# Optimization experiments

Measured on AMD Instinct MI355X. Metric: run time of the kernel, lower is better.

The kernel has to match this reference:

```python
import jax, jax.numpy as jnp
import numpy as np

BASE_TEMP, MIN_TEMP, MAX_TEMP = 0.07, 0.04, 0.2
B, D = 4096, 768


def setup_inputs() -> dict:
    key = jax.random.key(0)
    k1, k2, k3 = jax.random.split(key, 3)
    return {
        "vision_features": jax.random.normal(k1, (B, D), dtype=jnp.float32),
        "text_features": jax.random.normal(k2, (B, D), dtype=jnp.float32),
        "match_ids": jax.random.randint(k3, (B,), 0, 1024, dtype=jnp.int64),
    }


def reference(vision_features, text_features, match_ids):
    # L2-normalize features along the feature dim
    v = vision_features / jnp.linalg.norm(vision_features, axis=1, keepdims=True)
    t = text_features / jnp.linalg.norm(text_features, axis=1, keepdims=True)
    sim = v @ t.T  # [B, B]

    n = match_ids.shape[0]
    match = match_ids[:, None] == match_ids[None, :]  # [B, B] bool, diag True
    mf = match.astype(sim.dtype)
    eye = jnp.eye(n, dtype=sim.dtype)
    pos_mask = mf * (1.0 - eye)          # diagonal zeroed
    neg_mask = 1.0 - mf                   # diagonal also zero (was match)

    pos_mean = (pos_mask * sim).sum() / jnp.maximum(1.0, pos_mask.sum())
    neg_mean = (neg_mask * sim).sum() / jnp.maximum(1.0, neg_mask.sum())
    separation = pos_mean - neg_mean
    temp = jnp.clip(BASE_TEMP * (0.8 + 0.4 * jnp.exp(-2.0 * separation)),
                    MIN_TEMP, MAX_TEMP)

    logits = sim / temp
    # v2t: for each row i, sum over positives j of (-logits[i,j] + lse(row i))
    lse_rows = jax.nn.logsumexp(logits, axis=1)  # [B]
    v2t = (mf * (lse_rows[:, None] - logits)).sum()
    # t2v: for each column i, sum over positives j of (-logits[j,i] + lse(col i))
    lse_cols = jax.nn.logsumexp(logits, axis=0)  # [B]
    t2v = (mf * (lse_cols[None, :] - logits)).sum()

    num_pos = mf.sum()  # includes diagonal, matching the torch code
    v2t = v2t / num_pos
    t2v = t2v / num_pos
    loss = (v2t + t2v) / 2.0
    return loss
```

## Files before the change

### kernel.cpp

```cpp
#include <hip/hip_runtime.h>
#include <hip/hip_bf16.h>

#define NB 4096
#define DD 768
#define NKT 24
#define NBLK 256

typedef __bf16 bf16x8 __attribute__((ext_vector_type(8)));
typedef float f32x4 __attribute__((ext_vector_type(4)));
typedef unsigned int uint;

#define WAITVM(N) asm volatile("s_waitcnt vmcnt(" #N ")" ::: "memory")
#define WAITLGKM0 asm volatile("s_waitcnt lgkmcnt(0)" ::: "memory")

__global__ void init_kernel(float* scal)
{
    if (threadIdx.x < 16) scal[threadIdx.x] = 0.0f;
}

__device__ __forceinline__ void stage_range(
    __hip_bfloat16* ldsAll,
    const __hip_bfloat16* __restrict__ vhat, const __hip_bfloat16* __restrict__ that_,
    int rowBase, int colBase, int T, int i0, int i1, int wid, int lane)
{
    int u = T & 3;
    int k0 = T * 32;
    const __hip_bfloat16* src = (wid >= 4) ? that_ : vhat;
    int tb = (wid >= 4) ? colBase : rowBase;
    int w4 = wid & 3;
    int logc = (lane & 3) ^ ((lane >> 3) & 3);
    int rowIn = w4 * 64 + (lane >> 2);
    __hip_bfloat16* dbase = ldsAll + u * 16384 + ((wid >= 4) ? 8192 : 0) + w4 * 2048;
    #pragma unroll
    for (int i = i0; i <= i1; ++i) {
        const __hip_bfloat16* g = src + (size_t)(tb + rowIn + i * 16) * DD + k0 + logc * 8;
        __builtin_amdgcn_global_load_lds(
            (const __attribute__((address_space(1))) void*)g,
            (__attribute__((address_space(3))) void*)(dbase + i * 512),
            16, 0, 0);
    }
}

__global__ __launch_bounds__(512, 2) void fused_kernel(
    const float* __restrict__ vf, const float* __restrict__ tf, const int* __restrict__ ids,
    __hip_bfloat16* __restrict__ vhat, __hip_bfloat16* __restrict__ that_,
    float* scal, float* rs, float* cs, float* cntf, int* npart, uint* bar,
    float* __restrict__ out)
{
    __shared__ __hip_bfloat16 ldsAll[4 * 16384];
    __shared__ int idr[256], idc[256];
    __shared__ float red[24];
    __shared__ float rs_l[256], cs_l[256];
    __shared__ int bp[16], wred_i[8];
    __shared__ float ra[8], rn[8];
    __shared__ float invT_sh, mf_sh;

    int rawb = blockIdx.x;
    int t = threadIdx.x, wid = t >> 6, lane = t & 63;

    #pragma unroll
    for (int it = 0; it < 4; ++it) {
        int row = rawb * 32 + wid * 4 + it;
        const float* src;
        __hip_bfloat16* dst;
        if (row < NB) { src = vf + (size_t)row * DD; dst = vhat + (size_t)row * DD; }
        else          { src = tf + (size_t)(row - NB) * DD; dst = that_ + (size_t)(row - NB) * DD; }
        float4 x0 = *(const float4*)(src + lane * 4);
        float4 x1 = *(const float4*)(src + 256 + lane * 4);
        float4 x2 = *(const float4*)(src + 512 + lane * 4);
        float s = x0.x*x0.x + x0.y*x0.y + x0.z*x0.z + x0.w*x0.w
                + x1.x*x1.x + x1.y*x1.y + x1.z*x1.z + x1.w*x1.w
                + x2.x*x2.x + x2.y*x2.y + x2.z*x2.z + x2.w*x2.w;
        #pragma unroll
        for (int off = 1; off < 64; off <<= 1) s += __shfl_xor(s, off, 64);
        float scale = 1.0f / sqrtf(s);
        unsigned short* dsh = (unsigned short*)dst;
        ushort4 o0, o1, o2;
        o0.x = __builtin_bit_cast(unsigned short, __float2bfloat16(x0.x * scale));
        o0.y = __builtin_bit_cast(unsigned short, __float2bfloat16(x0.y * scale));
        o0.z = __builtin_bit_cast(unsigned short, __float2bfloat16(x0.z * scale));
        o0.w = __builtin_bit_cast(unsigned short, __float2bfloat16(x0.w * scale));
        o1.x = __builtin_bit_cast(unsigned short, __float2bfloat16(x1.x * scale));
        o1.y = __builtin_bit_cast(unsigned short, __float2bfloat16(x1.y * scale));
        o1.z = __builtin_bit_cast(unsigned short, __float2bfloat16(x1.z * scale));
        o1.w = __builtin_bit_cast(unsigned short, __float2bfloat16(x1.w * scale));
        o2.x = __builtin_bit_cast(unsigned short, __float2bfloat16(x2.x * scale));
        o2.y = __builtin_bit_cast(unsigned short, __float2bfloat16(x2.y * scale));
        o2.z = __builtin_bit_cast(unsigned short, __float2bfloat16(x2.z * scale));
        o2.w = __builtin_bit_cast(unsigned short, __float2bfloat16(x2.w * scale));
        *(ushort4*)(dsh + lane * 4)       = o0;
        *(ushort4*)(dsh + 256 + lane * 4) = o1;
        *(ushort4*)(dsh + 512 + lane * 4) = o2;
    }

    int* idsh = (int*)ldsAll;
    for (int i = t; i < NB; i += 512) idsh[i] = ids[i];
    __syncthreads();
    {
        int sub = t >> 5, l32 = t & 31;
        int my = idsh[rawb * 16 + sub];
        int c = 0;
        #pragma unroll 16
        for (int j = l32; j < NB; j += 32) c += (idsh[j] == my);
        #pragma unroll
        for (int off = 16; off > 0; off >>= 1) c += __shfl_down(c, off, 32);
        if (l32 == 0) { cntf[rawb * 16 + sub] = (float)c; bp[sub] = c; }
    }
    if (t < 32) rs[rawb * 32 + t] = 0.0f;
    __syncthreads();
    if (t == 0) {
        int s = 0;
        #pragma unroll
        for (int i = 0; i < 16; ++i) s += bp[i];
        npart[rawb] = s;
    }

    __syncthreads();
    if (t == 0) {
        __hip_atomic_fetch_add(bar, 1u, __ATOMIC_ACQ_REL, __HIP_MEMORY_SCOPE_AGENT);
        while (__hip_atomic_load(bar, __ATOMIC_ACQUIRE, __HIP_MEMORY_SCOPE_AGENT) < NBLK)
            __builtin_amdgcn_s_sleep(2);
    }
    __syncthreads();

    int rg = rawb & 7, sq = rawb >> 3;
    int by = (rg >> 1) * 4 + (sq >> 3);
    int bx = (rg & 1) * 8 + (sq & 7);
    int rowBase = by * 256, colBase = bx * 256;
    int wr = wid >> 2, wc = wid & 3;
    int fr = lane & 15, g = lane >> 4;

    f32x4 acc[8][4];
    #pragma unroll
    for (int m = 0; m < 8; ++m)
        #pragma unroll
        for (int n = 0; n < 4; ++n) acc[m][n] = (f32x4){0.f, 0.f, 0.f, 0.f};

    int pcoff = ((g ^ ((fr >> 1) & 3)) * 8);
    int aoff = (wr * 128 + fr) * 32 + pcoff;
    int boff = 8192 + (wc * 64 + fr) * 32 + pcoff;

    stage_range(ldsAll, vhat, that_, rowBase, colBase, 0, 0, 3, wid, lane);
    stage_range(ldsAll, vhat, that_, rowBase, colBase, 1, 0, 3, wid, lane);
    stage_range(ldsAll, vhat, that_, rowBase, colBase, 2, 0, 3, wid, lane);
    WAITVM(8);
    __builtin_amdgcn_s_barrier();

    for (int T = 0; T < NKT; ++T) {
        const __hip_bfloat16* U = ldsAll + (T & 3) * 16384;
        bf16x8 a0[4], bb[4];
        #pragma unroll
        for (int m = 0; m < 4; ++m) a0[m] = *(const bf16x8*)(U + aoff + m * 512);
        #pragma unroll
        for (int n = 0; n < 4; ++n) bb[n] = *(const bf16x8*)(U + boff + n * 512);
        if (T + 3 < NKT)
            stage_range(ldsAll, vhat, that_, rowBase, colBase, T + 3, 0, 1, wid, lane);
        __builtin_amdgcn_sched_barrier(0);
        __builtin_amdgcn_s_barrier();
        WAITLGKM0;
        __builtin_amdgcn_sched_barrier(0);
        __builtin_amdgcn_s_setprio(1);
        #pragma unroll
        for (int m = 0; m < 4; ++m)
            #pragma unroll
            for (int n = 0; n < 4; ++n)
                acc[m][n] = __builtin_amdgcn_mfma_f32_16x16x32_bf16(a0[m], bb[n], acc[m][n], 0, 0, 0);
        __builtin_amdgcn_s_setprio(0);
        __builtin_amdgcn_sched_barrier(0);
        __builtin_amdgcn_s_barrier();
        bf16x8 a1[4];
        #pragma unroll
        for (int m = 0; m < 4; ++m) a1[m] = *(const bf16x8*)(U + aoff + (m + 4) * 512);
        if (T + 3 < NKT)
            stage_range(ldsAll, vhat, that_, rowBase, colBase, T + 3, 2, 3, wid, lane);
        __builtin_amdgcn_sched_barrier(0);
        __builtin_amdgcn_s_barrier();
        WAITLGKM0;
        __builtin_amdgcn_sched_barrier(0);
        __builtin_amdgcn_s_setprio(1);
        #pragma unroll
        for (int m = 0; m < 4; ++m)
            #pragma unroll
            for (int n = 0; n < 4; ++n)
                acc[m + 4][n] = __builtin_amdgcn_mfma_f32_16x16x32_bf16(a1[m], bb[n], acc[m + 4][n], 0, 0, 0);
        __builtin_amdgcn_s_setprio(0);
        __builtin_amdgcn_sched_barrier(0);
        if (T < NKT - 3)       { WAITVM(8); }
        else if (T == NKT - 3) { WAITVM(4); }
        else if (T == NKT - 2) { WAITVM(0); }
        __builtin_amdgcn_s_barrier();
    }

    if (t < 256) idr[t] = ids[rowBase + t];
    else         idc[t - 256] = ids[colBase + (t - 256)];
    __syncthreads();
    {
        float tsum = 0.f, msum = 0.f, dsum = 0.f;
        #pragma unroll
        for (int m = 0; m < 8; ++m) {
            int rl = wr * 128 + m * 16 + g * 4;
            #pragma unroll
            for (int n = 0; n < 4; ++n) {
                int cl = wc * 64 + n * 16 + fr;
                int colId = idc[cl];
                int gj = colBase + cl;
                #pragma unroll
                for (int r = 0; r < 4; ++r) {
                    float val = acc[m][n][r];
                    tsum += val;
                    if (idr[rl + r] == colId) msum += val;
                    if (rowBase + rl + r == gj) dsum += val;
                }
            }
        }
        #pragma unroll
        for (int off = 32; off > 0; off >>= 1) {
            tsum += __shfl_down(tsum, off, 64);
            msum += __shfl_down(msum, off, 64);
            dsum += __shfl_down(dsum, off, 64);
        }
        if (lane == 0) { red[wid] = tsum; red[8 + wid] = msum; red[16 + wid] = dsum; }
        __syncthreads();
        if (t == 0) {
            float s0 = 0.f, s1 = 0.f, s2 = 0.f;
            #pragma unroll
            for (int w = 0; w < 8; ++w) { s0 += red[w]; s1 += red[8 + w]; s2 += red[16 + w]; }
            atomicAdd(&scal[0], s0);
            atomicAdd(&scal[1], s1);
            atomicAdd(&scal[2], s2);
        }
    }

    __syncthreads();
    if (t == 0) {
        __hip_atomic_fetch_add(bar, 1u, __ATOMIC_ACQ_REL, __HIP_MEMORY_SCOPE_AGENT);
        while (__hip_atomic_load(bar, __ATOMIC_ACQUIRE, __HIP_MEMORY_SCOPE_AGENT) < 2 * NBLK)
            __builtin_amdgcn_s_sleep(2);
    }
    __syncthreads();

    {
        int myn = (t < NBLK) ? npart[t] : 0;
        #pragma unroll
        for (int off = 32; off > 0; off >>= 1) myn += __shfl_down(myn, off, 64);
        if (lane == 0) wred_i[wid] = myn;
        __syncthreads();
        if (t == 0) {
            int npi = 0;
            #pragma unroll
            for (int w = 0; w < 8; ++w) npi += wred_i[w];
            float total = __hip_atomic_load(&scal[0], __ATOMIC_RELAXED, __HIP_MEMORY_SCOPE_AGENT);
            float mf    = __hip_atomic_load(&scal[1], __ATOMIC_RELAXED, __HIP_MEMORY_SCOPE_AGENT);
            float trace = __hip_atomic_load(&scal[2], __ATOMIC_RELAXED, __HIP_MEMORY_SCOPE_AGENT);
            float np = (float)npi;
            float pos_cnt = np - (float)NB;
            float neg_cnt = (float)NB * (float)NB - np;
            float pos_mean = (mf - trace) / fmaxf(1.0f, pos_cnt);
            float neg_mean = (total - mf) / fmaxf(1.0f, neg_cnt);
            float sep = pos_mean - neg_mean;
            float temp = 0.07f * (0.8f + 0.4f * expf(-2.0f * sep));
            temp = fminf(fmaxf(temp, 0.04f), 0.2f);
            invT_sh = 1.0f / temp;
            mf_sh = mf;
        }
        if (t < 256) { rs_l[t] = 0.0f; cs_l[t] = 0.0f; }
        __syncthreads();
    }
    float invT = invT_sh;

    #pragma unroll
    for (int m = 0; m < 8; ++m)
        #pragma unroll
        for (int n = 0; n < 4; ++n)
            #pragma unroll
            for (int r = 0; r < 4; ++r)
                acc[m][n][r] = __expf((acc[m][n][r] - 1.0f) * invT);
    #pragma unroll
    for (int m = 0; m < 8; ++m) {
        #pragma unroll
        for (int r = 0; r < 4; ++r) {
            float rp = 0.f;
            #pragma unroll
            for (int n = 0; n < 4; ++n) rp += acc[m][n][r];
            rp += __shfl_xor(rp, 1, 64);
            rp += __shfl_xor(rp, 2, 64);
            rp += __shfl_xor(rp, 4, 64);
            rp += __shfl_xor(rp, 8, 64);
            if (fr == 0) atomicAdd(&rs_l[wr * 128 + m * 16 + g * 4 + r], rp);
        }
    }
    #pragma unroll
    for (int n = 0; n < 4; ++n) {
        float cp = 0.f;
        #pragma unroll
        for (int m = 0; m < 8; ++m)
            #pragma unroll
            for (int r = 0; r < 4; ++r) cp += acc[m][n][r];
        cp += __shfl_xor(cp, 16, 64);
        cp += __shfl_xor(cp, 32, 64);
        if (g == 0) atomicAdd(&cs_l[wc * 64 + n * 16 + fr], cp);
    }
    __syncthreads();
    if (t < 256) {
        atomicAdd(&rs[rowBase + t], rs_l[t]);
        atomicAdd(&cs[colBase + t], cs_l[t]);
    }

    __syncthreads();
    if (t == 0)
        __hip_atomic_fetch_add(bar, 1u, __ATOMIC_ACQ_REL, __HIP_MEMORY_SCOPE_AGENT);
    if (rawb != 0) return;
    if (t == 0) {
        while (__hip_atomic_load(bar, __ATOMIC_ACQUIRE, __HIP_MEMORY_SCOPE_AGENT) < 3 * NBLK)
            __builtin_amdgcn_s_sleep(2);
    }
    __syncthreads();

    {
        float a = 0.f, npl = 0.f;
        for (int i = t; i < NB; i += 512) {
            float cf = cntf[i];
            a += cf * (logf(rs[i]) + logf(cs[i]));
            npl += cf;
        }
        #pragma unroll
        for (int off = 32; off > 0; off >>= 1) {
            a += __shfl_down(a, off, 64);
            npl += __shfl_down(npl, off, 64);
        }
        if (lane == 0) { ra[wid] = a; rn[wid] = npl; }
        __syncthreads();
        if (t == 0) {
            float A = 0.f, np = 0.f;
            #pragma unroll
            for (int w = 0; w < 8; ++w) { A += ra[w]; np += rn[w]; }
            out[0] = (A + 2.0f * invT_sh * (np - mf_sh)) / (2.0f * np);
        }
    }
}

extern "C" void kernel_launch(void* const* d_in, const int* in_sizes, int n_in,
                              void* d_out, int out_size, void* d_ws, size_t ws_size,
                              hipStream_t stream)
{
    const float* vf  = (const float*)d_in[0];
    const float* tf  = (const float*)d_in[1];
    const int*   ids = (const int*)d_in[2];

    float* ws_f = (float*)d_ws;
    float* scal = ws_f;
    float* rs   = ws_f + 16;
    float* cs   = ws_f + 16 + 4096;
    float* cntf = ws_f + 16 + 8192;
    int* npart  = (int*)(ws_f + 16 + 12288);
    uint* bar   = (uint*)(scal + 6);
    __hip_bfloat16* vhat  = (__hip_bfloat16*)((char*)d_ws + 131072);
    __hip_bfloat16* that_ = vhat + (size_t)NB * DD;

    init_kernel<<<1, 64, 0, stream>>>(scal);
    fused_kernel<<<NBLK, 512, 0, stream>>>(vf, tf, ids, vhat, that_,
                                           scal, rs, cs, cntf, npart, bar, (float*)d_out);
}
```

Measured before the change: 88.35 us.

## Collapse split-phase GEMM loop into single-barrier iteration with full-tile prefetch

Restructures the main bf16 MFMA k-loop so that each iteration issues the whole next-tile global-to-LDS prefetch up front, loads all A/B fragments, runs the 32 MFMAs, and synchronizes once. This replaces the previous two half-phases, which each used two barriers, explicit lgkmcnt waits and sched_barriers. The aim is to cut barrier and scheduling overhead and let the compiler interleave LDS reads with MFMAs. It also switches the normalization loads to nontemporal loads and vectorizes the match-id counting loop to int4 LDS reads. The cost is more live fragment registers and less explicit control over LDS/MFMA interleaving, which could hurt occupancy or the schedule.

New measurement: 95.60 us. 8.2% more time.

```diff
diff --git a/kernel.cpp b/kernel.cpp
--- a/kernel.cpp
+++ b/kernel.cpp
@@ -11,17 +11,16 @@
 typedef unsigned int uint;
 
 #define WAITVM(N) asm volatile("s_waitcnt vmcnt(" #N ")" ::: "memory")
-#define WAITLGKM0 asm volatile("s_waitcnt lgkmcnt(0)" ::: "memory")
 
 __global__ void init_kernel(float* scal)
 {
     if (threadIdx.x < 16) scal[threadIdx.x] = 0.0f;
 }
 
-__device__ __forceinline__ void stage_range(
+__device__ __forceinline__ void stage_tile(
     __hip_bfloat16* ldsAll,
     const __hip_bfloat16* __restrict__ vhat, const __hip_bfloat16* __restrict__ that_,
-    int rowBase, int colBase, int T, int i0, int i1, int wid, int lane)
+    int rowBase, int colBase, int T, int wid, int lane)
 {
     int u = T & 3;
     int k0 = T * 32;
@@ -32,7 +31,7 @@
     int rowIn = w4 * 64 + (lane >> 2);
     __hip_bfloat16* dbase = ldsAll + u * 16384 + ((wid >= 4) ? 8192 : 0) + w4 * 2048;
     #pragma unroll
-    for (int i = i0; i <= i1; ++i) {
+    for (int i = 0; i < 4; ++i) {
         const __hip_bfloat16* g = src + (size_t)(tb + rowIn + i * 16) * DD + k0 + logc * 8;
         __builtin_amdgcn_global_load_lds(
             (const __attribute__((address_space(1))) void*)g,
@@ -65,29 +64,29 @@
         __hip_bfloat16* dst;
         if (row < NB) { src = vf + (size_t)row * DD; dst = vhat + (size_t)row * DD; }
         else          { src = tf + (size_t)(row - NB) * DD; dst = that_ + (size_t)(row - NB) * DD; }
-        float4 x0 = *(const float4*)(src + lane * 4);
-        float4 x1 = *(const float4*)(src + 256 + lane * 4);
-        float4 x2 = *(const float4*)(src + 512 + lane * 4);
-        float s = x0.x*x0.x + x0.y*x0.y + x0.z*x0.z + x0.w*x0.w
-                + x1.x*x1.x + x1.y*x1.y + x1.z*x1.z + x1.w*x1.w
-                + x2.x*x2.x + x2.y*x2.y + x2.z*x2.z + x2.w*x2.w;
+        f32x4 x0 = __builtin_nontemporal_load((const f32x4*)(src + lane * 4));
+        f32x4 x1 = __builtin_nontemporal_load((const f32x4*)(src + 256 + lane * 4));
+        f32x4 x2 = __builtin_nontemporal_load((const f32x4*)(src + 512 + lane * 4));
+        float s = x0[0]*x0[0] + x0[1]*x0[1] + x0[2]*x0[2] + x0[3]*x0[3]
+                + x1[0]*x1[0] + x1[1]*x1[1] + x1[2]*x1[2] + x1[3]*x1[3]
+                + x2[0]*x2[0] + x2[1]*x2[1] + x2[2]*x2[2] + x2[3]*x2[3];
         #pragma unroll
         for (int off = 1; off < 64; off <<= 1) s += __shfl_xor(s, off, 64);
         float scale = 1.0f / sqrtf(s);
         unsigned short* dsh = (unsigned short*)dst;
         ushort4 o0, o1, o2;
-        o0.x = __builtin_bit_cast(unsigned short, __float2bfloat16(x0.x * scale));
-        o0.y = __builtin_bit_cast(unsigned short, __float2bfloat16(x0.y * scale));
-        o0.z = __builtin_bit_cast(unsigned short, __float2bfloat16(x0.z * scale));
-        o0.w = __builtin_bit_cast(unsigned short, __float2bfloat16(x0.w * scale));
-        o1.x = __builtin_bit_cast(unsigned short, __float2bfloat16(x1.x * scale));
-        o1.y = __builtin_bit_cast(unsigned short, __float2bfloat16(x1.y * scale));
-        o1.z = __builtin_bit_cast(unsigned short, __float2bfloat16(x1.z * scale));
-        o1.w = __builtin_bit_cast(unsigned short, __float2bfloat16(x1.w * scale));
-        o2.x = __builtin_bit_cast(unsigned short, __float2bfloat16(x2.x * scale));
-        o2.y = __builtin_bit_cast(unsigned short, __float2bfloat16(x2.y * scale));
-        o2.z = __builtin_bit_cast(unsigned short, __float2bfloat16(x2.z * scale));
-        o2.w = __builtin_bit_cast(unsigned short, __float2bfloat16(x2.w * scale));
+        o0.x = __builtin_bit_cast(unsigned short, __float2bfloat16(x0[0] * scale));
+        o0.y = __builtin_bit_cast(unsigned short, __float2bfloat16(x0[1] * scale));
+        o0.z = __builtin_bit_cast(unsigned short, __float2bfloat16(x0[2] * scale));
+        o0.w = __builtin_bit_cast(unsigned short, __float2bfloat16(x0[3] * scale));
+        o1.x = __builtin_bit_cast(unsigned short, __float2bfloat16(x1[0] * scale));
+        o1.y = __builtin_bit_cast(unsigned short, __float2bfloat16(x1[1] * scale));
+        o1.z = __builtin_bit_cast(unsigned short, __float2bfloat16(x1[2] * scale));
+        o1.w = __builtin_bit_cast(unsigned short, __float2bfloat16(x1[3] * scale));
+        o2.x = __builtin_bit_cast(unsigned short, __float2bfloat16(x2[0] * scale));
+        o2.y = __builtin_bit_cast(unsigned short, __float2bfloat16(x2[1] * scale));
+        o2.z = __builtin_bit_cast(unsigned short, __float2bfloat16(x2[2] * scale));
+        o2.w = __builtin_bit_cast(unsigned short, __float2bfloat16(x2[3] * scale));
         *(ushort4*)(dsh + lane * 4)       = o0;
         *(ushort4*)(dsh + 256 + lane * 4) = o1;
         *(ushort4*)(dsh + 512 + lane * 4) = o2;
@@ -99,9 +98,13 @@
     {
         int sub = t >> 5, l32 = t & 31;
         int my = idsh[rawb * 16 + sub];
+        const int4* idsh4 = (const int4*)idsh;
         int c = 0;
-        #pragma unroll 16
-        for (int j = l32; j < NB; j += 32) c += (idsh[j] == my);
+        #pragma unroll 8
+        for (int j = l32; j < NB / 4; j += 32) {
+            int4 v = idsh4[j];
+            c += (v.x == my) + (v.y == my) + (v.z == my) + (v.w == my);
+        }
         #pragma unroll
         for (int off = 16; off > 0; off >>= 1) c += __shfl_down(c, off, 32);
         if (l32 == 0) { cntf[rawb * 16 + sub] = (float)c; bp[sub] = c; }
@@ -140,51 +143,35 @@
     int aoff = (wr * 128 + fr) * 32 + pcoff;
     int boff = 8192 + (wc * 64 + fr) * 32 + pcoff;
 
-    stage_range(ldsAll, vhat, that_, rowBase, colBase, 0, 0, 3, wid, lane);
-    stage_range(ldsAll, vhat, that_, rowBase, colBase, 1, 0, 3, wid, lane);
-    stage_range(ldsAll, vhat, that_, rowBase, colBase, 2, 0, 3, wid, lane);
+    stage_tile(ldsAll, vhat, that_, rowBase, colBase, 0, wid, lane);
+    stage_tile(ldsAll, vhat, that_, rowBase, colBase, 1, wid, lane);
+    stage_tile(ldsAll, vhat, that_, rowBase, colBase, 2, wid, lane);
     WAITVM(8);
     __builtin_amdgcn_s_barrier();
 
     for (int T = 0; T < NKT; ++T) {
         const __hip_bfloat16* U = ldsAll + (T & 3) * 16384;
-        bf16x8 a0[4], bb[4];
+        if (T + 3 < NKT)
+            stage_tile(ldsAll, vhat, that_, rowBase, colBase, T + 3, wid, lane);
+        bf16x8 a0[4], bb[4], a1[4];
         #pragma unroll
         for (int m = 0; m < 4; ++m) a0[m] = *(const bf16x8*)(U + aoff + m * 512);
         #pragma unroll
         for (int n = 0; n < 4; ++n) bb[n] = *(const bf16x8*)(U + boff + n * 512);
-        if (T + 3 < NKT)
-            stage_range(ldsAll, vhat, that_, rowBase, colBase, T + 3, 0, 1, wid, lane);
-        __builtin_amdgcn_sched_barrier(0);
-        __builtin_amdgcn_s_barrier();
-        WAITLGKM0;
-        __builtin_amdgcn_sched_barrier(0);
+        #pragma unroll
+        for (int m = 0; m < 4; ++m) a1[m] = *(const bf16x8*)(U + aoff + (m + 4) * 512);
         __builtin_amdgcn_s_setprio(1);
         #pragma unroll
         for (int m = 0; m < 4; ++m)
             #pragma unroll
             for (int n = 0; n < 4; ++n)
                 acc[m][n] = __builtin_amdgcn_mfma_f32_16x16x32_bf16(a0[m], bb[n], acc[m][n], 0, 0, 0);
-        __builtin_amdgcn_s_setprio(0);
-        __builtin_amdgcn_sched_barrier(0);
-        __builtin_amdgcn_s_barrier();
-        bf16x8 a1[4];
-        #pragma unroll
-        for (int m = 0; m < 4; ++m) a1[m] = *(const bf16x8*)(U + aoff + (m + 4) * 512);
-        if (T + 3 < NKT)
-            stage_range(ldsAll, vhat, that_, rowBase, colBase, T + 3, 2, 3, wid, lane);
-        __builtin_amdgcn_sched_barrier(0);
-        __builtin_amdgcn_s_barrier();
-        WAITLGKM0;
-        __builtin_amdgcn_sched_barrier(0);
-        __builtin_amdgcn_s_setprio(1);
         #pragma unroll
         for (int m = 0; m < 4; ++m)
             #pragma unroll
             for (int n = 0; n < 4; ++n)
                 acc[m + 4][n] = __builtin_amdgcn_mfma_f32_16x16x32_bf16(a1[m], bb[n], acc[m + 4][n], 0, 0, 0);
         __builtin_amdgcn_s_setprio(0);
-        __builtin_amdgcn_sched_barrier(0);
         if (T < NKT - 3)       { WAITVM(8); }
         else if (T == NKT - 3) { WAITVM(4); }
         else if (T == NKT - 2) { WAITVM(0); }
```
